# Kernel tuning notes

Hardware: AMD Instinct MI355X
Metric: run time of the kernel (lower is better)

The kernel has to match this reference:

```python
import jax, jax.numpy as jnp
import numpy as np

B, L, K, H = 4, 256, 256, 768
KEY_SIZE, VAL_SIZE = 50000, 10000


def setup_inputs() -> dict:
    key = jax.random.key(0)
    k1, k2, k3, k4, k5, k6 = jax.random.split(key, 6)
    return {
        "hidden_state": jax.random.normal(k1, (B, L, H), dtype=jnp.float32),
        "key_seq": jax.random.randint(k2, (B, K), 0, KEY_SIZE),
        "value_matrix": jax.random.randint(k3, (B, L, K), 0, VAL_SIZE),
        "key_mask_matrix": jax.random.randint(k4, (B, L, K), 0, 2),
        "key_emb_table": jax.random.normal(k5, (KEY_SIZE, H), dtype=jnp.float32),
        "val_emb_table": jax.random.normal(k6, (VAL_SIZE, H), dtype=jnp.float32),
    }


def reference(hidden_state, key_seq, value_matrix, key_mask_matrix,
              key_emb_table, val_emb_table):
    temper = jnp.asarray(H, jnp.float32) ** 0.5
    # embedding lookups
    embedding_key = key_emb_table[key_seq]            # [B, K, H]
    embedding_val = val_emb_table[value_matrix]       # [B, L, K, H]
    # scores: hidden [B,L,H] x key [B,K,H] -> [B,L,K]
    u = jnp.einsum('blh,bkh->blk', hidden_state, embedding_key) / temper
    mask = jnp.clip(key_mask_matrix, 0, 1).astype(jnp.float32)
    delta_exp_u = jnp.exp(u) * mask                   # masked exp
    sum_delta = jnp.sum(delta_exp_u, axis=2, keepdims=True)
    p = delta_exp_u / (sum_delta + 1e-10)             # masked softmax [B,L,K]
    # weighted value sum (avoids the original's [H,B,L,K] broadcast+permute)
    o = jnp.einsum('blk,blkh->blh', p, embedding_val)
    return o + hidden_state
```

## Files before the change

kernel.cpp:

```cpp
#include <hip/hip_runtime.h>
#include <math.h>

typedef float    f32x2 __attribute__((ext_vector_type(2)));
typedef float    f32x4 __attribute__((ext_vector_type(4)));
typedef _Float16 f16x2 __attribute__((ext_vector_type(2)));

static constexpr int B_ = 4;
static constexpr int L_ = 256;
static constexpr int K_ = 256;
static constexpr int H_ = 768;
static constexpr int H2_ = H_ / 2;
static constexpr int VAL_SIZE_ = 10000;
static constexpr float INV_TEMPER = 0.03608439182435161f;

__device__ __forceinline__ unsigned pack_f16x2(float a, float b) {
  f16x2 p = {(_Float16)a, (_Float16)b};
  return __builtin_bit_cast(unsigned, p);
}
__device__ __forceinline__ float fdot2u(unsigned a, unsigned b, float c) {
#if __has_builtin(__builtin_amdgcn_fdot2)
  return __builtin_amdgcn_fdot2(__builtin_bit_cast(f16x2, a),
                                __builtin_bit_cast(f16x2, b), c, false);
#else
  f16x2 va = __builtin_bit_cast(f16x2, a);
  f16x2 vb = __builtin_bit_cast(f16x2, b);
  return c + (float)va.x * (float)vb.x + (float)va.y * (float)vb.y;
#endif
}

__device__ __forceinline__ float4 nt_load4(const float* p) {
  f32x4 v = __builtin_nontemporal_load(reinterpret_cast<const f32x4*>(p));
  return make_float4(v.x, v.y, v.z, v.w);
}

#if __has_builtin(__builtin_amdgcn_cvt_pk_fp8_f32)
#define HW_FP8_ENC 1
#endif
#if __has_builtin(__builtin_amdgcn_cvt_pk_f32_fp8)
#define HW_FP8_DEC 1
#endif

__device__ __forceinline__ unsigned fp8_enc1(float f) {
  unsigned s = (__float_as_uint(f) >> 31) << 7;
  float af = fminf(fabsf(f), 448.0f);
  unsigned em;
  if (af < 0.015625f) {
    em = (unsigned)rintf(af * 512.0f);
  } else {
    unsigned m = __float_as_uint(af);
    m += 0x7ffffu + ((m >> 20) & 1u);
    em = (m >> 20) - (120u << 3);
  }
  return s | em;
}
__device__ __forceinline__ float fp8_dec1(unsigned b) {
  unsigned em = b & 0x7fu;
  unsigned sbit = (b & 0x80u) << 24;
  float n = __uint_as_float(sbit | ((em + 960u) << 20));
  float sub = __uint_as_float(sbit | 0x3F800000u) * (float)em * 0.001953125f;
  return em >= 8u ? n : sub;
}
__device__ __forceinline__ unsigned fp8_enc4(float a, float b, float c, float d) {
#ifdef HW_FP8_ENC
  int w = 0;
  w = __builtin_amdgcn_cvt_pk_fp8_f32(a, b, w, false);
  w = __builtin_amdgcn_cvt_pk_fp8_f32(c, d, w, true);
  return (unsigned)w;
#else
  return fp8_enc1(a) | (fp8_enc1(b) << 8) | (fp8_enc1(c) << 16) | (fp8_enc1(d) << 24);
#endif
}
__device__ __forceinline__ void fp8_dec4(unsigned w, float* o) {
#ifdef HW_FP8_DEC
  f32x2 lo = __builtin_amdgcn_cvt_pk_f32_fp8((int)w, false);
  f32x2 hi = __builtin_amdgcn_cvt_pk_f32_fp8((int)w, true);
  o[0] = lo.x; o[1] = lo.y; o[2] = hi.x; o[3] = hi.y;
#else
  o[0] = fp8_dec1(w & 0xffu);
  o[1] = fp8_dec1((w >> 8) & 0xffu);
  o[2] = fp8_dec1((w >> 16) & 0xffu);
  o[3] = fp8_dec1(w >> 24);
#endif
}

static constexpr int TBLK = (K_ / 64) * (H_ / 64) * B_;
static constexpr int SBLK = (L_ / 2) * B_;
static constexpr int CBLK = (VAL_SIZE_ * H_) / 4096;

__global__ __launch_bounds__(256)
void k_prep(const int* __restrict__ key_seq,
            const float* __restrict__ key_emb,
            const float* __restrict__ vtab,
            unsigned* __restrict__ ET2,
            unsigned char* __restrict__ VT8) {
  __shared__ float tile[64][65];
  const int t = threadIdx.x;

  if (blockIdx.x >= TBLK) {
    const size_t base = (size_t)(blockIdx.x - TBLK) * 4096;
#pragma unroll
    for (int c = 0; c < 4; ++c) {
      const size_t e0 = base + (size_t)c * 1024 + (size_t)t * 4;
      const float4 a = nt_load4(vtab + e0);
      *reinterpret_cast<unsigned*>(VT8 + e0) = fp8_enc4(a.x, a.y, a.z, a.w);
    }
    return;
  }

  const int blk  = blockIdx.x;
  const int kb   = (blk % (K_ / 64)) * 64;
  const int hb   = ((blk / (K_ / 64)) % (H_ / 64)) * 64;
  const int b    = blk / ((K_ / 64) * (H_ / 64));
  const int sub  = t >> 6;
  const int lane = t & 63;

#pragma unroll
  for (int p = 0; p < 16; ++p) {
    const int kl  = p * 4 + sub;
    const int row = key_seq[b * K_ + kb + kl];
    tile[kl][lane] = key_emb[(size_t)row * H_ + hb + lane];
  }
  __syncthreads();
#pragma unroll
  for (int p = 0; p < 8; ++p) {
    const int hl2 = p * 4 + sub;
    ET2[((size_t)b * H2_ + (hb >> 1) + hl2) * K_ + kb + lane] =
        pack_f16x2(tile[lane][2 * hl2], tile[lane][2 * hl2 + 1]);
  }
}

__global__ __launch_bounds__(512)
void k_scores_pv(const float* __restrict__ hidden,
                 const unsigned* __restrict__ ET2,
                 const int* __restrict__ mask,
                 const int* __restrict__ vmat,
                 const unsigned char* __restrict__ VT8,
                 float* __restrict__ out) {
  __shared__ unsigned hid2[2 * H2_];
  __shared__ float4   part[2][512];
  __shared__ int      vmat_lds[2][K_];
  __shared__ float    pw[2][K_];
  __shared__ int      vidx[2][K_];
  __shared__ float    osum[2][2][H_];
  __shared__ int      nrow[2];

  const int t  = threadIdx.x;
  const int l0 = (blockIdx.x & 127) * 2;
  const int b  = blockIdx.x >> 7;

  const float* hsrc = hidden + ((size_t)b * L_ + l0) * H_;
  for (int i = t; i < 2 * H2_; i += 512) {
    const float2 hv = *reinterpret_cast<const float2*>(hsrc + 2 * i);
    hid2[i] = pack_f16x2(hv.x, hv.y);
  }
  if (t >= 256 && t < 384) {
    const int i  = t - 256;
    const int r  = i >> 6;
    const int c4 = (i & 63) * 4;
    *reinterpret_cast<int4*>(&vmat_lds[r][c4]) =
        *reinterpret_cast<const int4*>(vmat + ((size_t)b * L_ + l0 + r) * K_ + c4);
  }
  __syncthreads();

  {
    const int kq = t & 63;
    const int hq = t >> 6;
    float4 acc[2];
#pragma unroll
    for (int l = 0; l < 2; ++l) acc[l] = make_float4(0.f, 0.f, 0.f, 0.f);

    const unsigned* etp =
        ET2 + (size_t)b * H2_ * K_ + (size_t)(hq * 48) * K_ + kq * 4;
    const int hbase2 = hq * 48;
#pragma unroll 4
    for (int hh = 0; hh < 48; ++hh) {
      const uint4 e = *reinterpret_cast<const uint4*>(etp + (size_t)hh * K_);
#pragma unroll
      for (int l = 0; l < 2; ++l) {
        const unsigned hv2 = hid2[l * H2_ + hbase2 + hh];
        acc[l].x = fdot2u(e.x, hv2, acc[l].x);
        acc[l].y = fdot2u(e.y, hv2, acc[l].y);
        acc[l].z = fdot2u(e.z, hv2, acc[l].z);
        acc[l].w = fdot2u(e.w, hv2, acc[l].w);
      }
    }
#pragma unroll
    for (int l = 0; l < 2; ++l) part[l][t] = acc[l];
  }
  __syncthreads();

  if (t < 128) {
    const int kq2 = t & 63;
    const int l2  = t >> 6;
    float4 a = part[l2][kq2];
#pragma unroll
    for (int c = 1; c < 8; ++c) {
      const float4 pc = part[l2][c * 64 + kq2];
      a.x += pc.x; a.y += pc.y; a.z += pc.z; a.w += pc.w;
    }

    const int lrow = l0 + l2;
    const int4 m4 = *reinterpret_cast<const int4*>(
        mask + ((size_t)b * L_ + lrow) * K_ + kq2 * 4);
    float ex[4];
    ex[0] = (m4.x > 0) ? expf(a.x * INV_TEMPER) : 0.f;
    ex[1] = (m4.y > 0) ? expf(a.y * INV_TEMPER) : 0.f;
    ex[2] = (m4.z > 0) ? expf(a.z * INV_TEMPER) : 0.f;
    ex[3] = (m4.w > 0) ? expf(a.w * INV_TEMPER) : 0.f;

    float s = ex[0] + ex[1] + ex[2] + ex[3];
#pragma unroll
    for (int off = 32; off > 0; off >>= 1) s += __shfl_down(s, off);
    const float tot = __shfl(s, 0) + 1e-10f;
    const float rtot = 1.0f / tot;

    const unsigned long long lt = (1ull << kq2) - 1ull;
    unsigned long long m[4];
    int run = 0;
    int pos[4];
#pragma unroll
    for (int cc = 0; cc < 4; ++cc) {
      m[cc] = __ballot(ex[cc] != 0.f);
      pos[cc] = run + (int)__popcll(m[cc] & lt);
      run += (int)__popcll(m[cc]);
    }
#pragma unroll
    for (int cc = 0; cc < 4; ++cc) {
      if (ex[cc] != 0.f) {
        pw[l2][pos[cc]]   = ex[cc] * rtot;
        vidx[l2][pos[cc]] = vmat_lds[l2][kq2 * 4 + cc];
      }
    }
    if (kq2 == 0) nrow[l2] = run;
  }
  __syncthreads();

  const int w    = t >> 6;
  const int lane = t & 63;
  const int r    = w & 1;
  const int q    = w >> 1;
  const int n    = nrow[r];

  float acc[12];
#pragma unroll
  for (int i = 0; i < 12; ++i) acc[i] = 0.f;

#pragma unroll 4
  for (int j = q; j < n; j += 4) {
    const float wgt = pw[r][j];
    const int   idx = vidx[r][j];
    const uint3 v = *reinterpret_cast<const uint3*>(
        VT8 + (size_t)idx * H_ + lane * 12);
    float f[12];
    fp8_dec4(v.x, f);
    fp8_dec4(v.y, f + 4);
    fp8_dec4(v.z, f + 8);
#pragma unroll
    for (int i = 0; i < 12; ++i) acc[i] += wgt * f[i];
  }

  if (q < 2) {
#pragma unroll
    for (int c = 0; c < 3; ++c)
      *reinterpret_cast<float4*>(&osum[r][q][lane * 12 + c * 4]) =
          make_float4(acc[c * 4], acc[c * 4 + 1], acc[c * 4 + 2], acc[c * 4 + 3]);
  }
  __syncthreads();
  if (q >= 2) {
#pragma unroll
    for (int i = 0; i < 12; ++i) osum[r][q - 2][lane * 12 + i] += acc[i];
  }
  __syncthreads();

  if (q == 0) {
    const float* hrow = hidden + ((size_t)b * L_ + l0 + r) * H_;
    float*       orow = out    + ((size_t)b * L_ + l0 + r) * H_;
#pragma unroll
    for (int c = 0; c < 3; ++c) {
      const int h0 = c * 256 + lane * 4;
      const float4 o0 = *reinterpret_cast<const float4*>(&osum[r][0][h0]);
      const float4 o1 = *reinterpret_cast<const float4*>(&osum[r][1][h0]);
      const float4 hv = *reinterpret_cast<const float4*>(hrow + h0);
      *reinterpret_cast<float4*>(orow + h0) =
          make_float4(o0.x + o1.x + hv.x, o0.y + o1.y + hv.y,
                      o0.z + o1.z + hv.z, o0.w + o1.w + hv.w);
    }
  }
}

extern "C" void kernel_launch(void* const* d_in, const int* in_sizes, int n_in,
                              void* d_out, int out_size, void* d_ws, size_t ws_size,
                              hipStream_t stream) {
  (void)in_sizes; (void)n_in; (void)out_size; (void)ws_size;
  const float* hidden  = (const float*)d_in[0];
  const int*   key_seq = (const int*)d_in[1];
  const int*   vmat    = (const int*)d_in[2];
  const int*   mask    = (const int*)d_in[3];
  const float* key_emb = (const float*)d_in[4];
  const float* val_emb = (const float*)d_in[5];
  float* out = (float*)d_out;

  unsigned char* VT8 = (unsigned char*)d_ws;
  unsigned*      ET2 = (unsigned*)(VT8 + (size_t)VAL_SIZE_ * H_);

  k_prep<<<TBLK + CBLK, 256, 0, stream>>>(key_seq, key_emb, val_emb, ET2, VT8);
  k_scores_pv<<<SBLK, 512, 0, stream>>>(hidden, ET2, mask, vmat, VT8, out);
}
```

Before: 35.06 us.

## Overlap value-table FP8 conversion with score computation via grid-wide counter

Moves the value-table FP32→FP8 conversion out of the prep kernel and into two spare waves of each fused scores/PV block. Those waves convert the table while six waves compute the scores, and a global atomic counter with a spin-wait gates the PV phase until every conversion slice is done. The score reduction is re-split across six waves of 64 h-pairs instead of eight of 48. The gain depends on all 512 blocks being co-resident, which is checked with an occupancy query. The design adds a memset launch and a risk of deadlock or spin overhead if residency assumptions fail.

```diff
diff --git a/kernel.cpp b/kernel.cpp
--- a/kernel.cpp
+++ b/kernel.cpp
@@ -84,8 +84,12 @@
 }
 
 static constexpr int TBLK = (K_ / 64) * (H_ / 64) * B_;
-static constexpr int SBLK = (L_ / 2) * B_;
 static constexpr int CBLK = (VAL_SIZE_ * H_) / 4096;
+static constexpr int FBLK = (L_ / 2) * B_;
+static constexpr int NCONV_SIG = 2 * FBLK;
+static constexpr size_t VT8_BYTES = (size_t)VAL_SIZE_ * H_;
+static constexpr size_t ET2_BYTES = (size_t)B_ * H2_ * K_ * 4;
+static constexpr size_t CTR_OFF   = VT8_BYTES + ET2_BYTES;
 
 __global__ __launch_bounds__(256)
 void k_prep(const int* __restrict__ key_seq,
@@ -129,55 +133,58 @@
   }
 }
 
-__global__ __launch_bounds__(512)
-void k_scores_pv(const float* __restrict__ hidden,
-                 const unsigned* __restrict__ ET2,
-                 const int* __restrict__ mask,
-                 const int* __restrict__ vmat,
-                 const unsigned char* __restrict__ VT8,
-                 float* __restrict__ out) {
+__global__ __launch_bounds__(512, 4)
+void k_fused(const float* __restrict__ hidden,
+             const unsigned* __restrict__ ET2,
+             const int* __restrict__ mask,
+             const int* __restrict__ vmat,
+             const float* __restrict__ vtab,
+             unsigned char* __restrict__ VT8,
+             float* __restrict__ out,
+             unsigned* __restrict__ ctr,
+             const int gated) {
   __shared__ unsigned hid2[2 * H2_];
-  __shared__ float4   part[2][512];
+  __shared__ float4   part[2][6][64];
   __shared__ int      vmat_lds[2][K_];
   __shared__ float    pw[2][K_];
   __shared__ int      vidx[2][K_];
   __shared__ float    osum[2][2][H_];
   __shared__ int      nrow[2];
 
-  const int t  = threadIdx.x;
-  const int l0 = (blockIdx.x & 127) * 2;
-  const int b  = blockIdx.x >> 7;
-
-  const float* hsrc = hidden + ((size_t)b * L_ + l0) * H_;
-  for (int i = t; i < 2 * H2_; i += 512) {
-    const float2 hv = *reinterpret_cast<const float2*>(hsrc + 2 * i);
-    hid2[i] = pack_f16x2(hv.x, hv.y);
-  }
-  if (t >= 256 && t < 384) {
-    const int i  = t - 256;
-    const int r  = i >> 6;
-    const int c4 = (i & 63) * 4;
-    *reinterpret_cast<int4*>(&vmat_lds[r][c4]) =
-        *reinterpret_cast<const int4*>(vmat + ((size_t)b * L_ + l0 + r) * K_ + c4);
-  }
-  __syncthreads();
-
-  {
-    const int kq = t & 63;
-    const int hq = t >> 6;
+  const int t    = threadIdx.x;
+  const int wave = t >> 6;
+  const int lane = t & 63;
+  const int l0   = ((int)blockIdx.x & 127) * 2;
+  const int b    = (int)blockIdx.x >> 7;
+
+  if (wave < 6) {
+    const int hq = wave;
+    const float* hsrc = hidden + ((size_t)b * L_ + l0) * H_;
+#pragma unroll
+    for (int l = 0; l < 2; ++l) {
+      const float2 hv = *reinterpret_cast<const float2*>(
+          hsrc + l * H_ + (hq * 64 + lane) * 2);
+      hid2[l * H2_ + hq * 64 + lane] = pack_f16x2(hv.x, hv.y);
+    }
+    if (t < 128) {
+      const int r  = t >> 6;
+      const int c4 = lane * 4;
+      *reinterpret_cast<int4*>(&vmat_lds[r][c4]) =
+          *reinterpret_cast<const int4*>(
+              vmat + ((size_t)b * L_ + l0 + r) * K_ + c4);
+    }
+
     float4 acc[2];
 #pragma unroll
     for (int l = 0; l < 2; ++l) acc[l] = make_float4(0.f, 0.f, 0.f, 0.f);
-
     const unsigned* etp =
-        ET2 + (size_t)b * H2_ * K_ + (size_t)(hq * 48) * K_ + kq * 4;
-    const int hbase2 = hq * 48;
+        ET2 + (size_t)b * H2_ * K_ + (size_t)(hq * 64) * K_ + lane * 4;
 #pragma unroll 4
-    for (int hh = 0; hh < 48; ++hh) {
+    for (int hh = 0; hh < 64; ++hh) {
       const uint4 e = *reinterpret_cast<const uint4*>(etp + (size_t)hh * K_);
 #pragma unroll
       for (int l = 0; l < 2; ++l) {
-        const unsigned hv2 = hid2[l * H2_ + hbase2 + hh];
+        const unsigned hv2 = hid2[l * H2_ + hq * 64 + hh];
         acc[l].x = fdot2u(e.x, hv2, acc[l].x);
         acc[l].y = fdot2u(e.y, hv2, acc[l].y);
         acc[l].z = fdot2u(e.z, hv2, acc[l].z);
@@ -185,17 +192,37 @@
       }
     }
 #pragma unroll
-    for (int l = 0; l < 2; ++l) part[l][t] = acc[l];
+    for (int l = 0; l < 2; ++l) part[l][hq][lane] = acc[l];
+  } else if (gated) {
+    const int s0 = (int)blockIdx.x + (wave == 7 ? FBLK : 0);
+#pragma unroll
+    for (int rep = 0; rep < 2; ++rep) {
+      const int s = s0 + rep * 2 * FBLK;
+      if (s < CBLK) {
+        const size_t base4 = (size_t)s * 1024;
+#pragma unroll
+        for (int i = 0; i < 16; ++i) {
+          const size_t idx4 = base4 + (size_t)i * 64 + lane;
+          const float4 a = nt_load4(vtab + idx4 * 4);
+          *reinterpret_cast<unsigned*>(VT8 + idx4 * 4) =
+              fp8_enc4(a.x, a.y, a.z, a.w);
+        }
+      }
+    }
+    __threadfence();
+    if (lane == 0)
+      __hip_atomic_fetch_add(ctr, 1u, __ATOMIC_RELEASE,
+                             __HIP_MEMORY_SCOPE_AGENT);
   }
   __syncthreads();
 
   if (t < 128) {
-    const int kq2 = t & 63;
+    const int kq2 = lane;
     const int l2  = t >> 6;
-    float4 a = part[l2][kq2];
-#pragma unroll
-    for (int c = 1; c < 8; ++c) {
-      const float4 pc = part[l2][c * 64 + kq2];
+    float4 a = part[l2][0][kq2];
+#pragma unroll
+    for (int c = 1; c < 6; ++c) {
+      const float4 pc = part[l2][c][kq2];
       a.x += pc.x; a.y += pc.y; a.z += pc.z; a.w += pc.w;
     }
 
@@ -233,13 +260,17 @@
     }
     if (kq2 == 0) nrow[l2] = run;
   }
-  __syncthreads();
-
-  const int w    = t >> 6;
-  const int lane = t & 63;
-  const int r    = w & 1;
-  const int q    = w >> 1;
-  const int n    = nrow[r];
+
+  if (gated) {
+    while (__hip_atomic_load(ctr, __ATOMIC_ACQUIRE,
+                             __HIP_MEMORY_SCOPE_AGENT) < (unsigned)NCONV_SIG)
+      __builtin_amdgcn_s_sleep(2);
+  }
+  __syncthreads();
+
+  const int r = wave & 1;
+  const int q = wave >> 1;
+  const int n = nrow[r];
 
   float acc[12];
 #pragma unroll
@@ -301,8 +332,21 @@
   float* out = (float*)d_out;
 
   unsigned char* VT8 = (unsigned char*)d_ws;
-  unsigned*      ET2 = (unsigned*)(VT8 + (size_t)VAL_SIZE_ * H_);
-
-  k_prep<<<TBLK + CBLK, 256, 0, stream>>>(key_seq, key_emb, val_emb, ET2, VT8);
-  k_scores_pv<<<SBLK, 512, 0, stream>>>(hidden, ET2, mask, vmat, VT8, out);
-}
+  unsigned*      ET2 = (unsigned*)(VT8 + VT8_BYTES);
+  unsigned*      ctr = (unsigned*)((char*)d_ws + CTR_OFF);
+
+  int occ = 0;
+  hipError_t e = hipOccupancyMaxActiveBlocksPerMultiprocessor(&occ, k_fused, 512, 0);
+  const bool gated = (e == hipSuccess && occ >= 2);
+
+  hipMemsetAsync(ctr, 0, 64, stream);
+  if (gated) {
+    k_prep<<<TBLK, 256, 0, stream>>>(key_seq, key_emb, val_emb, ET2, VT8);
+    k_fused<<<FBLK, 512, 0, stream>>>(hidden, ET2, mask, vmat, val_emb, VT8,
+                                      out, ctr, 1);
+  } else {
+    k_prep<<<TBLK + CBLK, 256, 0, stream>>>(key_seq, key_emb, val_emb, ET2, VT8);
+    k_fused<<<FBLK, 512, 0, stream>>>(hidden, ET2, mask, vmat, val_emb, VT8,
+                                      out, ctr, 0);
+  }
+}
```

Result: slower. 40.10 us (+14.4%).

## Split pipeline into three kernels, overlapping fp8 table conversion with scoring

Applied to the files above, without the earlier changes.

Moves the value-table fp8 conversion out of the key-gather prep kernel and into the scoring kernel's grid, so table conversion overlaps with score computation instead of delaying it. The PV accumulation becomes its own kernel with one row per block and 8 waves, fed by compacted weights and indices staged through global workspace. This raises parallelism in the gather-heavy PV phase, at the cost of an extra launch and a round-trip of softmax weights and indices through global memory.

```diff
diff --git a/kernel.cpp b/kernel.cpp
--- a/kernel.cpp
+++ b/kernel.cpp
@@ -86,31 +86,21 @@
 static constexpr int TBLK = (K_ / 64) * (H_ / 64) * B_;
 static constexpr int SBLK = (L_ / 2) * B_;
 static constexpr int CBLK = (VAL_SIZE_ * H_) / 4096;
+static constexpr size_t VT8_BYTES = (size_t)VAL_SIZE_ * H_;
+static constexpr size_t ET2_BYTES = (size_t)B_ * H2_ * K_ * 4;
+static constexpr size_t PW_BYTES  = (size_t)B_ * L_ * K_ * 4;
+static constexpr size_t VX_BYTES  = PW_BYTES;
 
 __global__ __launch_bounds__(256)
-void k_prep(const int* __restrict__ key_seq,
-            const float* __restrict__ key_emb,
-            const float* __restrict__ vtab,
-            unsigned* __restrict__ ET2,
-            unsigned char* __restrict__ VT8) {
+void k_gather_keys_T(const int* __restrict__ key_seq,
+                     const float* __restrict__ key_emb,
+                     unsigned* __restrict__ ET2) {
   __shared__ float tile[64][65];
-  const int t = threadIdx.x;
-
-  if (blockIdx.x >= TBLK) {
-    const size_t base = (size_t)(blockIdx.x - TBLK) * 4096;
-#pragma unroll
-    for (int c = 0; c < 4; ++c) {
-      const size_t e0 = base + (size_t)c * 1024 + (size_t)t * 4;
-      const float4 a = nt_load4(vtab + e0);
-      *reinterpret_cast<unsigned*>(VT8 + e0) = fp8_enc4(a.x, a.y, a.z, a.w);
-    }
-    return;
-  }
-
   const int blk  = blockIdx.x;
   const int kb   = (blk % (K_ / 64)) * 64;
   const int hb   = ((blk / (K_ / 64)) % (H_ / 64)) * 64;
   const int b    = blk / ((K_ / 64) * (H_ / 64));
+  const int t    = threadIdx.x;
   const int sub  = t >> 6;
   const int lane = t & 63;
 
@@ -130,54 +120,66 @@
 }
 
 __global__ __launch_bounds__(512)
-void k_scores_pv(const float* __restrict__ hidden,
-                 const unsigned* __restrict__ ET2,
-                 const int* __restrict__ mask,
-                 const int* __restrict__ vmat,
-                 const unsigned char* __restrict__ VT8,
-                 float* __restrict__ out) {
+void k_scores_conv(const float* __restrict__ hidden,
+                   const unsigned* __restrict__ ET2,
+                   const int* __restrict__ mask,
+                   const int* __restrict__ vmat,
+                   const float* __restrict__ vtab,
+                   unsigned char* __restrict__ VT8,
+                   float* __restrict__ Pw,
+                   int* __restrict__ Vx,
+                   int* __restrict__ nrowG) {
   __shared__ unsigned hid2[2 * H2_];
-  __shared__ float4   part[2][512];
+  __shared__ float4   part[2][8][64];
   __shared__ int      vmat_lds[2][K_];
-  __shared__ float    pw[2][K_];
-  __shared__ int      vidx[2][K_];
-  __shared__ float    osum[2][2][H_];
-  __shared__ int      nrow[2];
-
-  const int t  = threadIdx.x;
-  const int l0 = (blockIdx.x & 127) * 2;
-  const int b  = blockIdx.x >> 7;
+  __shared__ float    pw_l[2][K_];
+  __shared__ int      vx_l[2][K_];
+  __shared__ int      nrow_l[2];
+
+  const int t = threadIdx.x;
+
+  if (blockIdx.x >= SBLK) {
+    const size_t base = (size_t)(blockIdx.x - SBLK) * 4096;
+#pragma unroll
+    for (int c = 0; c < 2; ++c) {
+      const size_t e0 = base + (size_t)c * 2048 + (size_t)t * 4;
+      const float4 a = nt_load4(vtab + e0);
+      *reinterpret_cast<unsigned*>(VT8 + e0) = fp8_enc4(a.x, a.y, a.z, a.w);
+    }
+    return;
+  }
+
+  const int wave = t >> 6;
+  const int lane = t & 63;
+  const int l0   = ((int)blockIdx.x & 127) * 2;
+  const int b    = (int)blockIdx.x >> 7;
 
   const float* hsrc = hidden + ((size_t)b * L_ + l0) * H_;
   for (int i = t; i < 2 * H2_; i += 512) {
     const float2 hv = *reinterpret_cast<const float2*>(hsrc + 2 * i);
     hid2[i] = pack_f16x2(hv.x, hv.y);
   }
-  if (t >= 256 && t < 384) {
-    const int i  = t - 256;
-    const int r  = i >> 6;
-    const int c4 = (i & 63) * 4;
+  if (t < 128) {
+    const int r  = t >> 6;
+    const int c4 = lane * 4;
     *reinterpret_cast<int4*>(&vmat_lds[r][c4]) =
         *reinterpret_cast<const int4*>(vmat + ((size_t)b * L_ + l0 + r) * K_ + c4);
   }
   __syncthreads();
 
   {
-    const int kq = t & 63;
-    const int hq = t >> 6;
+    const int hq = wave;
     float4 acc[2];
 #pragma unroll
     for (int l = 0; l < 2; ++l) acc[l] = make_float4(0.f, 0.f, 0.f, 0.f);
-
     const unsigned* etp =
-        ET2 + (size_t)b * H2_ * K_ + (size_t)(hq * 48) * K_ + kq * 4;
-    const int hbase2 = hq * 48;
+        ET2 + (size_t)b * H2_ * K_ + (size_t)(hq * 48) * K_ + lane * 4;
 #pragma unroll 4
     for (int hh = 0; hh < 48; ++hh) {
       const uint4 e = *reinterpret_cast<const uint4*>(etp + (size_t)hh * K_);
 #pragma unroll
       for (int l = 0; l < 2; ++l) {
-        const unsigned hv2 = hid2[l * H2_ + hbase2 + hh];
+        const unsigned hv2 = hid2[l * H2_ + hq * 48 + hh];
         acc[l].x = fdot2u(e.x, hv2, acc[l].x);
         acc[l].y = fdot2u(e.y, hv2, acc[l].y);
         acc[l].z = fdot2u(e.z, hv2, acc[l].z);
@@ -185,17 +187,17 @@
       }
     }
 #pragma unroll
-    for (int l = 0; l < 2; ++l) part[l][t] = acc[l];
+    for (int l = 0; l < 2; ++l) part[l][hq][lane] = acc[l];
   }
   __syncthreads();
 
   if (t < 128) {
-    const int kq2 = t & 63;
+    const int kq2 = lane;
     const int l2  = t >> 6;
-    float4 a = part[l2][kq2];
+    float4 a = part[l2][0][kq2];
 #pragma unroll
     for (int c = 1; c < 8; ++c) {
-      const float4 pc = part[l2][c * 64 + kq2];
+      const float4 pc = part[l2][c][kq2];
       a.x += pc.x; a.y += pc.y; a.z += pc.z; a.w += pc.w;
     }
 
@@ -224,31 +226,71 @@
       pos[cc] = run + (int)__popcll(m[cc] & lt);
       run += (int)__popcll(m[cc]);
     }
+    pw_l[l2][kq2] = 0.f; pw_l[l2][64 + kq2] = 0.f;
+    pw_l[l2][128 + kq2] = 0.f; pw_l[l2][192 + kq2] = 0.f;
 #pragma unroll
     for (int cc = 0; cc < 4; ++cc) {
       if (ex[cc] != 0.f) {
-        pw[l2][pos[cc]]   = ex[cc] * rtot;
-        vidx[l2][pos[cc]] = vmat_lds[l2][kq2 * 4 + cc];
+        pw_l[l2][pos[cc]] = ex[cc] * rtot;
+        vx_l[l2][pos[cc]] = vmat_lds[l2][kq2 * 4 + cc];
       }
     }
-    if (kq2 == 0) nrow[l2] = run;
-  }
-  __syncthreads();
-
-  const int w    = t >> 6;
+    if (kq2 == 0) nrow_l[l2] = run;
+  }
+  __syncthreads();
+
+  if (t < 128) {
+    const int r  = t >> 6;
+    const int c4 = lane * 4;
+    const size_t go = ((size_t)b * L_ + l0 + r) * K_ + c4;
+    *reinterpret_cast<float4*>(Pw + go) =
+        *reinterpret_cast<const float4*>(&pw_l[r][c4]);
+    *reinterpret_cast<int4*>(Vx + go) =
+        *reinterpret_cast<const int4*>(&vx_l[r][c4]);
+    if (lane == 0) nrowG[b * L_ + l0 + r] = nrow_l[r];
+  }
+}
+
+__global__ __launch_bounds__(512)
+void k_pv_add(const float* __restrict__ hidden,
+              const float* __restrict__ Pw,
+              const int* __restrict__ Vx,
+              const int* __restrict__ nrowG,
+              const unsigned char* __restrict__ VT8,
+              float* __restrict__ out) {
+  __shared__ float pw[K_];
+  __shared__ int   vx[K_];
+  __shared__ float osum[4][H_];
+  __shared__ int   nn;
+
+  const int bid  = blockIdx.x;
+  const int l    = bid & 255;
+  const int b    = bid >> 8;
+  const int t    = threadIdx.x;
+  const int wave = t >> 6;
   const int lane = t & 63;
-  const int r    = w & 1;
-  const int q    = w >> 1;
-  const int n    = nrow[r];
-
+  const size_t go = ((size_t)b * L_ + l) * K_;
+
+  if (t < 64) {
+    *reinterpret_cast<float4*>(&pw[t * 4]) =
+        *reinterpret_cast<const float4*>(Pw + go + t * 4);
+  } else if (t < 128) {
+    *reinterpret_cast<int4*>(&vx[(t - 64) * 4]) =
+        *reinterpret_cast<const int4*>(Vx + go + (t - 64) * 4);
+  } else if (t == 128) {
+    nn = nrowG[b * L_ + l];
+  }
+  __syncthreads();
+
+  const int n = nn;
   float acc[12];
 #pragma unroll
   for (int i = 0; i < 12; ++i) acc[i] = 0.f;
 
 #pragma unroll 4
-  for (int j = q; j < n; j += 4) {
-    const float wgt = pw[r][j];
-    const int   idx = vidx[r][j];
+  for (int j = wave; j < n; j += 8) {
+    const float wgt = pw[j];
+    const int   idx = vx[j];
     const uint3 v = *reinterpret_cast<const uint3*>(
         VT8 + (size_t)idx * H_ + lane * 12);
     float f[12];
@@ -259,27 +301,32 @@
     for (int i = 0; i < 12; ++i) acc[i] += wgt * f[i];
   }
 
-  if (q < 2) {
+  if (wave < 4) {
 #pragma unroll
     for (int c = 0; c < 3; ++c)
-      *reinterpret_cast<float4*>(&osum[r][q][lane * 12 + c * 4]) =
+      *reinterpret_cast<float4*>(&osum[wave][lane * 12 + c * 4]) =
           make_float4(acc[c * 4], acc[c * 4 + 1], acc[c * 4 + 2], acc[c * 4 + 3]);
   }
   __syncthreads();
-  if (q >= 2) {
-#pragma unroll
-    for (int i = 0; i < 12; ++i) osum[r][q - 2][lane * 12 + i] += acc[i];
-  }
-  __syncthreads();
-
-  if (q == 0) {
-    const float* hrow = hidden + ((size_t)b * L_ + l0 + r) * H_;
-    float*       orow = out    + ((size_t)b * L_ + l0 + r) * H_;
+  if (wave >= 4) {
+#pragma unroll
+    for (int i = 0; i < 12; ++i) osum[wave - 4][lane * 12 + i] += acc[i];
+  }
+  __syncthreads();
+  if (wave < 2) {
+#pragma unroll
+    for (int i = 0; i < 12; ++i) osum[wave][lane * 12 + i] += osum[wave + 2][lane * 12 + i];
+  }
+  __syncthreads();
+
+  if (wave == 0) {
+    const float* hrow = hidden + ((size_t)b * L_ + l) * H_;
+    float*       orow = out    + ((size_t)b * L_ + l) * H_;
 #pragma unroll
     for (int c = 0; c < 3; ++c) {
       const int h0 = c * 256 + lane * 4;
-      const float4 o0 = *reinterpret_cast<const float4*>(&osum[r][0][h0]);
-      const float4 o1 = *reinterpret_cast<const float4*>(&osum[r][1][h0]);
+      const float4 o0 = *reinterpret_cast<const float4*>(&osum[0][h0]);
+      const float4 o1 = *reinterpret_cast<const float4*>(&osum[1][h0]);
       const float4 hv = *reinterpret_cast<const float4*>(hrow + h0);
       *reinterpret_cast<float4*>(orow + h0) =
           make_float4(o0.x + o1.x + hv.x, o0.y + o1.y + hv.y,
@@ -300,9 +347,14 @@
   const float* val_emb = (const float*)d_in[5];
   float* out = (float*)d_out;
 
-  unsigned char* VT8 = (unsigned char*)d_ws;
-  unsigned*      ET2 = (unsigned*)(VT8 + (size_t)VAL_SIZE_ * H_);
-
-  k_prep<<<TBLK + CBLK, 256, 0, stream>>>(key_seq, key_emb, val_emb, ET2, VT8);
-  k_scores_pv<<<SBLK, 512, 0, stream>>>(hidden, ET2, mask, vmat, VT8, out);
-}
+  unsigned char* VT8   = (unsigned char*)d_ws;
+  unsigned*      ET2   = (unsigned*)(VT8 + VT8_BYTES);
+  float*         Pw    = (float*)((char*)ET2 + ET2_BYTES);
+  int*           Vx    = (int*)((char*)Pw + PW_BYTES);
+  int*           nrowG = (int*)((char*)Vx + VX_BYTES);
+
+  k_gather_keys_T<<<TBLK, 256, 0, stream>>>(key_seq, key_emb, ET2);
+  k_scores_conv<<<SBLK + CBLK, 512, 0, stream>>>(hidden, ET2, mask, vmat,
+                                                 val_emb, VT8, Pw, Vx, nrowG);
+  k_pv_add<<<B_ * L_, 512, 0, stream>>>(hidden, Pw, Vx, nrowG, VT8, out);
+}
```

Measured after the change: 38.39 us. 9.5% more time.

## Fuse prep and scores/PV kernels into one cooperative kernel with grid sync

Applied to the files above, without the earlier changes.

Merges the table-conversion/key-transpose prep kernel and the scores+weighted-value kernel into a single cooperative launch separated by a grid-wide barrier. The intent is to remove the second kernel launch and its gap. The fp8 conversion is spread across all 512 blocks with a grid-stride loop. The cost is per-call host queries for device attributes and occupancy, the grid sync itself, and heavier LDS use per block that could cap occupancy. A fallback keeps the two-kernel path when a cooperative launch is not possible.

```diff
diff --git a/kernel.cpp b/kernel.cpp
--- a/kernel.cpp
+++ b/kernel.cpp
@@ -1,5 +1,8 @@
 #include <hip/hip_runtime.h>
+#include <hip/hip_cooperative_groups.h>
 #include <math.h>
+
+namespace cg = cooperative_groups;
 
 typedef float    f32x2 __attribute__((ext_vector_type(2)));
 typedef float    f32x4 __attribute__((ext_vector_type(4)));
@@ -84,8 +87,231 @@
 }
 
 static constexpr int TBLK = (K_ / 64) * (H_ / 64) * B_;
-static constexpr int SBLK = (L_ / 2) * B_;
+static constexpr int FBLK = (L_ / 2) * B_;
 static constexpr int CBLK = (VAL_SIZE_ * H_) / 4096;
+static constexpr int CVT_WORDS = VAL_SIZE_ * H_ / 4;
+static constexpr size_t VT8_BYTES = (size_t)VAL_SIZE_ * H_;
+static constexpr size_t ET2_BYTES = (size_t)B_ * H2_ * K_ * 4;
+
+struct SharedP2 {
+  unsigned hid2[2 * H2_];
+  float4   part[2][8][64];
+  int      vmat_lds[2][K_];
+  float    pw[2][K_];
+  int      vidx[2][K_];
+  float    osum[2][2][H_];
+  int      nrow[2];
+};
+
+__device__ __forceinline__ void phase2(SharedP2& s,
+                                       const float* __restrict__ hidden,
+                                       const unsigned* __restrict__ ET2,
+                                       const int* __restrict__ mask,
+                                       const int* __restrict__ vmat,
+                                       const unsigned char* __restrict__ VT8,
+                                       float* __restrict__ out,
+                                       const int b, const int l0) {
+  const int t    = threadIdx.x;
+  const int wave = t >> 6;
+  const int lane = t & 63;
+
+  const float* hsrc = hidden + ((size_t)b * L_ + l0) * H_;
+  for (int i = t; i < 2 * H2_; i += 512) {
+    const float2 hv = *reinterpret_cast<const float2*>(hsrc + 2 * i);
+    s.hid2[i] = pack_f16x2(hv.x, hv.y);
+  }
+  if (t < 128) {
+    const int r  = t >> 6;
+    const int c4 = lane * 4;
+    *reinterpret_cast<int4*>(&s.vmat_lds[r][c4]) =
+        *reinterpret_cast<const int4*>(vmat + ((size_t)b * L_ + l0 + r) * K_ + c4);
+  }
+  __syncthreads();
+
+  {
+    float4 acc0 = make_float4(0.f, 0.f, 0.f, 0.f);
+    float4 acc1 = make_float4(0.f, 0.f, 0.f, 0.f);
+    const unsigned* etp =
+        ET2 + (size_t)b * H2_ * K_ + (size_t)(wave * 48) * K_ + lane * 4;
+#pragma unroll 4
+    for (int hh = 0; hh < 48; ++hh) {
+      const uint4 e = *reinterpret_cast<const uint4*>(etp + (size_t)hh * K_);
+      const unsigned h0 = s.hid2[wave * 48 + hh];
+      const unsigned h1 = s.hid2[H2_ + wave * 48 + hh];
+      acc0.x = fdot2u(e.x, h0, acc0.x);
+      acc0.y = fdot2u(e.y, h0, acc0.y);
+      acc0.z = fdot2u(e.z, h0, acc0.z);
+      acc0.w = fdot2u(e.w, h0, acc0.w);
+      acc1.x = fdot2u(e.x, h1, acc1.x);
+      acc1.y = fdot2u(e.y, h1, acc1.y);
+      acc1.z = fdot2u(e.z, h1, acc1.z);
+      acc1.w = fdot2u(e.w, h1, acc1.w);
+    }
+    s.part[0][wave][lane] = acc0;
+    s.part[1][wave][lane] = acc1;
+  }
+  __syncthreads();
+
+  if (t < 128) {
+    const int kq2 = lane;
+    const int l2  = t >> 6;
+    float4 a = s.part[l2][0][kq2];
+#pragma unroll
+    for (int c = 1; c < 8; ++c) {
+      const float4 pc = s.part[l2][c][kq2];
+      a.x += pc.x; a.y += pc.y; a.z += pc.z; a.w += pc.w;
+    }
+
+    const int lrow = l0 + l2;
+    const int4 m4 = *reinterpret_cast<const int4*>(
+        mask + ((size_t)b * L_ + lrow) * K_ + kq2 * 4);
+    float ex[4];
+    ex[0] = (m4.x > 0) ? expf(a.x * INV_TEMPER) : 0.f;
+    ex[1] = (m4.y > 0) ? expf(a.y * INV_TEMPER) : 0.f;
+    ex[2] = (m4.z > 0) ? expf(a.z * INV_TEMPER) : 0.f;
+    ex[3] = (m4.w > 0) ? expf(a.w * INV_TEMPER) : 0.f;
+
+    float sm = ex[0] + ex[1] + ex[2] + ex[3];
+#pragma unroll
+    for (int off = 32; off > 0; off >>= 1) sm += __shfl_down(sm, off);
+    const float tot = __shfl(sm, 0) + 1e-10f;
+    const float rtot = 1.0f / tot;
+
+    const unsigned long long lt = (1ull << kq2) - 1ull;
+    unsigned long long m[4];
+    int run = 0;
+    int pos[4];
+#pragma unroll
+    for (int cc = 0; cc < 4; ++cc) {
+      m[cc] = __ballot(ex[cc] != 0.f);
+      pos[cc] = run + (int)__popcll(m[cc] & lt);
+      run += (int)__popcll(m[cc]);
+    }
+#pragma unroll
+    for (int cc = 0; cc < 4; ++cc) {
+      if (ex[cc] != 0.f) {
+        s.pw[l2][pos[cc]]   = ex[cc] * rtot;
+        s.vidx[l2][pos[cc]] = s.vmat_lds[l2][kq2 * 4 + cc];
+      }
+    }
+    if (kq2 == 0) s.nrow[l2] = run;
+  }
+  __syncthreads();
+
+  const int r = wave & 1;
+  const int q = wave >> 1;
+  const int n = s.nrow[r];
+
+  float acc[12];
+#pragma unroll
+  for (int i = 0; i < 12; ++i) acc[i] = 0.f;
+
+#pragma unroll 4
+  for (int j = q; j < n; j += 4) {
+    const float wgt = s.pw[r][j];
+    const int   idx = s.vidx[r][j];
+    const uint3 v = *reinterpret_cast<const uint3*>(
+        VT8 + (size_t)idx * H_ + lane * 12);
+    float f[12];
+    fp8_dec4(v.x, f);
+    fp8_dec4(v.y, f + 4);
+    fp8_dec4(v.z, f + 8);
+#pragma unroll
+    for (int i = 0; i < 12; ++i) acc[i] += wgt * f[i];
+  }
+
+  if (q < 2) {
+#pragma unroll
+    for (int c = 0; c < 3; ++c)
+      *reinterpret_cast<float4*>(&s.osum[r][q][lane * 12 + c * 4]) =
+          make_float4(acc[c * 4], acc[c * 4 + 1], acc[c * 4 + 2], acc[c * 4 + 3]);
+  }
+  __syncthreads();
+  if (q >= 2) {
+#pragma unroll
+    for (int i = 0; i < 12; ++i) s.osum[r][q - 2][lane * 12 + i] += acc[i];
+  }
+  __syncthreads();
+
+  if (q == 0) {
+    const float* hrow = hidden + ((size_t)b * L_ + l0 + r) * H_;
+    float*       orow = out    + ((size_t)b * L_ + l0 + r) * H_;
+#pragma unroll
+    for (int c = 0; c < 3; ++c) {
+      const int h0 = c * 256 + lane * 4;
+      const float4 o0 = *reinterpret_cast<const float4*>(&s.osum[r][0][h0]);
+      const float4 o1 = *reinterpret_cast<const float4*>(&s.osum[r][1][h0]);
+      const float4 hv = *reinterpret_cast<const float4*>(hrow + h0);
+      *reinterpret_cast<float4*>(orow + h0) =
+          make_float4(o0.x + o1.x + hv.x, o0.y + o1.y + hv.y,
+                      o0.z + o1.z + hv.z, o0.w + o1.w + hv.w);
+    }
+  }
+}
+
+__global__ __launch_bounds__(512, 4)
+void k_all(const float* __restrict__ hidden,
+           const int* __restrict__ key_seq,
+           const int* __restrict__ vmat,
+           const int* __restrict__ mask,
+           const float* __restrict__ key_emb,
+           const float* __restrict__ vtab,
+           unsigned* __restrict__ ET2,
+           unsigned char* __restrict__ VT8,
+           float* __restrict__ out) {
+  __shared__ float    tile[64][65];
+  __shared__ SharedP2 s2;
+
+  const int t    = threadIdx.x;
+  const int bid  = blockIdx.x;
+  const int lane = t & 63;
+
+  {
+    const int gtid = bid * 512 + t;
+#pragma unroll
+    for (int i = 0; i < 8; ++i) {
+      const int w = i * (FBLK * 512) + gtid;
+      if (w < CVT_WORDS) {
+        const float4 a = nt_load4(vtab + (size_t)w * 4);
+        *reinterpret_cast<unsigned*>(VT8 + (size_t)w * 4) =
+            fp8_enc4(a.x, a.y, a.z, a.w);
+      }
+    }
+  }
+
+  if (bid < TBLK && t < 256) {
+    const int kb  = (bid % (K_ / 64)) * 64;
+    const int hb  = ((bid / (K_ / 64)) % (H_ / 64)) * 64;
+    const int bb  = bid / ((K_ / 64) * (H_ / 64));
+    const int sub = t >> 6;
+#pragma unroll
+    for (int p = 0; p < 16; ++p) {
+      const int kl  = p * 4 + sub;
+      const int row = key_seq[bb * K_ + kb + kl];
+      tile[kl][lane] = key_emb[(size_t)row * H_ + hb + lane];
+    }
+  }
+  __syncthreads();
+  if (bid < TBLK && t < 256) {
+    const int kb  = (bid % (K_ / 64)) * 64;
+    const int hb  = ((bid / (K_ / 64)) % (H_ / 64)) * 64;
+    const int bb  = bid / ((K_ / 64) * (H_ / 64));
+    const int sub = t >> 6;
+#pragma unroll
+    for (int p = 0; p < 8; ++p) {
+      const int hl2 = p * 4 + sub;
+      ET2[((size_t)bb * H2_ + (hb >> 1) + hl2) * K_ + kb + lane] =
+          pack_f16x2(tile[lane][2 * hl2], tile[lane][2 * hl2 + 1]);
+    }
+  }
+
+  __threadfence();
+  cg::this_grid().sync();
+
+  const int l0 = (bid & 127) * 2;
+  const int b  = bid >> 7;
+  phase2(s2, hidden, ET2, mask, vmat, VT8, out, b, l0);
+}
 
 __global__ __launch_bounds__(256)
 void k_prep(const int* __restrict__ key_seq,
@@ -129,163 +355,17 @@
   }
 }
 
-__global__ __launch_bounds__(512)
-void k_scores_pv(const float* __restrict__ hidden,
-                 const unsigned* __restrict__ ET2,
-                 const int* __restrict__ mask,
-                 const int* __restrict__ vmat,
-                 const unsigned char* __restrict__ VT8,
-                 float* __restrict__ out) {
-  __shared__ unsigned hid2[2 * H2_];
-  __shared__ float4   part[2][512];
-  __shared__ int      vmat_lds[2][K_];
-  __shared__ float    pw[2][K_];
-  __shared__ int      vidx[2][K_];
-  __shared__ float    osum[2][2][H_];
-  __shared__ int      nrow[2];
-
-  const int t  = threadIdx.x;
-  const int l0 = (blockIdx.x & 127) * 2;
-  const int b  = blockIdx.x >> 7;
-
-  const float* hsrc = hidden + ((size_t)b * L_ + l0) * H_;
-  for (int i = t; i < 2 * H2_; i += 512) {
-    const float2 hv = *reinterpret_cast<const float2*>(hsrc + 2 * i);
-    hid2[i] = pack_f16x2(hv.x, hv.y);
-  }
-  if (t >= 256 && t < 384) {
-    const int i  = t - 256;
-    const int r  = i >> 6;
-    const int c4 = (i & 63) * 4;
-    *reinterpret_cast<int4*>(&vmat_lds[r][c4]) =
-        *reinterpret_cast<const int4*>(vmat + ((size_t)b * L_ + l0 + r) * K_ + c4);
-  }
-  __syncthreads();
-
-  {
-    const int kq = t & 63;
-    const int hq = t >> 6;
-    float4 acc[2];
-#pragma unroll
-    for (int l = 0; l < 2; ++l) acc[l] = make_float4(0.f, 0.f, 0.f, 0.f);
-
-    const unsigned* etp =
-        ET2 + (size_t)b * H2_ * K_ + (size_t)(hq * 48) * K_ + kq * 4;
-    const int hbase2 = hq * 48;
-#pragma unroll 4
-    for (int hh = 0; hh < 48; ++hh) {
-      const uint4 e = *reinterpret_cast<const uint4*>(etp + (size_t)hh * K_);
-#pragma unroll
-      for (int l = 0; l < 2; ++l) {
-        const unsigned hv2 = hid2[l * H2_ + hbase2 + hh];
-        acc[l].x = fdot2u(e.x, hv2, acc[l].x);
-        acc[l].y = fdot2u(e.y, hv2, acc[l].y);
-        acc[l].z = fdot2u(e.z, hv2, acc[l].z);
-        acc[l].w = fdot2u(e.w, hv2, acc[l].w);
-      }
-    }
-#pragma unroll
-    for (int l = 0; l < 2; ++l) part[l][t] = acc[l];
-  }
-  __syncthreads();
-
-  if (t < 128) {
-    const int kq2 = t & 63;
-    const int l2  = t >> 6;
-    float4 a = part[l2][kq2];
-#pragma unroll
-    for (int c = 1; c < 8; ++c) {
-      const float4 pc = part[l2][c * 64 + kq2];
-      a.x += pc.x; a.y += pc.y; a.z += pc.z; a.w += pc.w;
-    }
-
-    const int lrow = l0 + l2;
-    const int4 m4 = *reinterpret_cast<const int4*>(
-        mask + ((size_t)b * L_ + lrow) * K_ + kq2 * 4);
-    float ex[4];
-    ex[0] = (m4.x > 0) ? expf(a.x * INV_TEMPER) : 0.f;
-    ex[1] = (m4.y > 0) ? expf(a.y * INV_TEMPER) : 0.f;
-    ex[2] = (m4.z > 0) ? expf(a.z * INV_TEMPER) : 0.f;
-    ex[3] = (m4.w > 0) ? expf(a.w * INV_TEMPER) : 0.f;
-
-    float s = ex[0] + ex[1] + ex[2] + ex[3];
-#pragma unroll
-    for (int off = 32; off > 0; off >>= 1) s += __shfl_down(s, off);
-    const float tot = __shfl(s, 0) + 1e-10f;
-    const float rtot = 1.0f / tot;
-
-    const unsigned long long lt = (1ull << kq2) - 1ull;
-    unsigned long long m[4];
-    int run = 0;
-    int pos[4];
-#pragma unroll
-    for (int cc = 0; cc < 4; ++cc) {
-      m[cc] = __ballot(ex[cc] != 0.f);
-      pos[cc] = run + (int)__popcll(m[cc] & lt);
-      run += (int)__popcll(m[cc]);
-    }
-#pragma unroll
-    for (int cc = 0; cc < 4; ++cc) {
-      if (ex[cc] != 0.f) {
-        pw[l2][pos[cc]]   = ex[cc] * rtot;
-        vidx[l2][pos[cc]] = vmat_lds[l2][kq2 * 4 + cc];
-      }
-    }
-    if (kq2 == 0) nrow[l2] = run;
-  }
-  __syncthreads();
-
-  const int w    = t >> 6;
-  const int lane = t & 63;
-  const int r    = w & 1;
-  const int q    = w >> 1;
-  const int n    = nrow[r];
-
-  float acc[12];
-#pragma unroll
-  for (int i = 0; i < 12; ++i) acc[i] = 0.f;
-
-#pragma unroll 4
-  for (int j = q; j < n; j += 4) {
-    const float wgt = pw[r][j];
-    const int   idx = vidx[r][j];
-    const uint3 v = *reinterpret_cast<const uint3*>(
-        VT8 + (size_t)idx * H_ + lane * 12);
-    float f[12];
-    fp8_dec4(v.x, f);
-    fp8_dec4(v.y, f + 4);
-    fp8_dec4(v.z, f + 8);
-#pragma unroll
-    for (int i = 0; i < 12; ++i) acc[i] += wgt * f[i];
-  }
-
-  if (q < 2) {
-#pragma unroll
-    for (int c = 0; c < 3; ++c)
-      *reinterpret_cast<float4*>(&osum[r][q][lane * 12 + c * 4]) =
-          make_float4(acc[c * 4], acc[c * 4 + 1], acc[c * 4 + 2], acc[c * 4 + 3]);
-  }
-  __syncthreads();
-  if (q >= 2) {
-#pragma unroll
-    for (int i = 0; i < 12; ++i) osum[r][q - 2][lane * 12 + i] += acc[i];
-  }
-  __syncthreads();
-
-  if (q == 0) {
-    const float* hrow = hidden + ((size_t)b * L_ + l0 + r) * H_;
-    float*       orow = out    + ((size_t)b * L_ + l0 + r) * H_;
-#pragma unroll
-    for (int c = 0; c < 3; ++c) {
-      const int h0 = c * 256 + lane * 4;
-      const float4 o0 = *reinterpret_cast<const float4*>(&osum[r][0][h0]);
-      const float4 o1 = *reinterpret_cast<const float4*>(&osum[r][1][h0]);
-      const float4 hv = *reinterpret_cast<const float4*>(hrow + h0);
-      *reinterpret_cast<float4*>(orow + h0) =
-          make_float4(o0.x + o1.x + hv.x, o0.y + o1.y + hv.y,
-                      o0.z + o1.z + hv.z, o0.w + o1.w + hv.w);
-    }
-  }
+__global__ __launch_bounds__(512, 4)
+void k_fused2(const float* __restrict__ hidden,
+              const unsigned* __restrict__ ET2,
+              const int* __restrict__ mask,
+              const int* __restrict__ vmat,
+              const unsigned char* __restrict__ VT8,
+              float* __restrict__ out) {
+  __shared__ SharedP2 s2;
+  const int l0 = ((int)blockIdx.x & 127) * 2;
+  const int b  = (int)blockIdx.x >> 7;
+  phase2(s2, hidden, ET2, mask, vmat, VT8, out, b, l0);
 }
 
 extern "C" void kernel_launch(void* const* d_in, const int* in_sizes, int n_in,
@@ -297,12 +377,30 @@
   const int*   vmat    = (const int*)d_in[2];
   const int*   mask    = (const int*)d_in[3];
   const float* key_emb = (const float*)d_in[4];
-  const float* val_emb = (const float*)d_in[5];
+  const float* vtab    = (const float*)d_in[5];
   float* out = (float*)d_out;
 
   unsigned char* VT8 = (unsigned char*)d_ws;
-  unsigned*      ET2 = (unsigned*)(VT8 + (size_t)VAL_SIZE_ * H_);
-
-  k_prep<<<TBLK + CBLK, 256, 0, stream>>>(key_seq, key_emb, val_emb, ET2, VT8);
-  k_scores_pv<<<SBLK, 512, 0, stream>>>(hidden, ET2, mask, vmat, VT8, out);
-}
+  unsigned*      ET2 = (unsigned*)(VT8 + VT8_BYTES);
+
+  int dev = 0;
+  hipGetDevice(&dev);
+  int coop = 0;
+  hipDeviceGetAttribute(&coop, hipDeviceAttributeCooperativeLaunch, dev);
+  int occ = 0;
+  hipError_t oe = hipOccupancyMaxActiveBlocksPerMultiprocessor(&occ, k_all, 512, 0);
+
+  bool done = false;
+  if (coop && oe == hipSuccess && occ >= 2) {
+    void* args[] = {(void*)&hidden, (void*)&key_seq, (void*)&vmat, (void*)&mask,
+                    (void*)&key_emb, (void*)&vtab, (void*)&ET2, (void*)&VT8,
+                    (void*)&out};
+    hipError_t le = hipLaunchCooperativeKernel((const void*)k_all, dim3(FBLK),
+                                               dim3(512), args, 0u, stream);
+    done = (le == hipSuccess);
+  }
+  if (!done) {
+    k_prep<<<TBLK + CBLK, 256, 0, stream>>>(key_seq, key_emb, vtab, ET2, VT8);
+    k_fused2<<<FBLK, 512, 0, stream>>>(hidden, ET2, mask, vmat, VT8, out);
+  }
+}
```

Result: no change. 35.11 us (+0.1%).
